# Kernel optimization log

Measured on AMD Instinct MI355X. Metric: run time of the kernel, lower is better.

Reference implementation:

```python
import jax, jax.numpy as jnp
import numpy as np

TEMPERATURE = 0.05


def setup_inputs() -> dict:
    key = jax.random.key(0)
    k1, k2 = jax.random.split(key)
    B, D = 4096, 1024
    # scale 0.1 keeps pairwise distances O(3) so the original exp(-d/T) is sane
    text_embeddings = 0.1 * jax.random.normal(k1, (B, D), dtype=jnp.float32)
    image_embeddings = 0.1 * jax.random.normal(k2, (B, D), dtype=jnp.float32)
    positive_pairs = jnp.arange(B, dtype=jnp.int32)  # unused by the loss body
    return {
        "text_embeddings": text_embeddings,
        "image_embeddings": image_embeddings,
        "positive_pairs": positive_pairs,
    }


def _pairwise_l2(t, m):
    # ||t_i - m_j|| via GEMM expansion; [B, B]
    sq = (
        jnp.sum(t * t, axis=1, keepdims=True)
        + jnp.sum(m * m, axis=1)[None, :]
        - 2.0 * (t @ m.T)
    )
    return jnp.sqrt(jnp.maximum(sq, 0.0))


def reference(text_embeddings, image_embeddings, positive_pairs):
    # loss_i = -log( exp(-d_ii/T) / sum_{j != i} exp(-d_ij/T) )
    #        = logsumexp_{j != i}(-d_ij/T) + d_ii/T   (exact same math, stable)
    dist = _pairwise_l2(text_embeddings, image_embeddings)  # [B, B]
    logits = -dist / TEMPERATURE
    diag = jnp.diagonal(logits)  # log numerator per row
    B = logits.shape[0]
    eye = jnp.eye(B, dtype=bool)
    masked = jnp.where(eye, -jnp.inf, logits)  # exclude self-term from denom
    lse = jax.nn.logsumexp(masked, axis=1)
    return jnp.mean(lse - diag)
```

## Files before the change

kernel.cpp:

```cpp
#include <hip/hip_runtime.h>
#include <math.h>


#define NB 4096
#define ND 1024
#define LSE_BIAS 90.0f
#define A2 28.85390082f
#define C2 129.8425537f

typedef short short8 __attribute__((ext_vector_type(8)));
typedef unsigned short ushort4v __attribute__((ext_vector_type(4)));
typedef float f32x4 __attribute__((ext_vector_type(4)));

__device__ inline unsigned short f2bf(float f) {
  unsigned int u = __float_as_uint(f);
  u = (u + 0x7FFFu + ((u >> 16) & 1u)) >> 16;
  return (unsigned short)u;
}

__device__ inline void gload_lds16(const unsigned short* g, unsigned short* l) {
  __builtin_amdgcn_global_load_lds(
      (const __attribute__((address_space(1))) unsigned int*)g,
      (__attribute__((address_space(3))) unsigned int*)l, 16, 0, 0);
}

__global__ void prep_kernel(const float* __restrict__ T, const float* __restrict__ M,
                            unsigned short* __restrict__ tb, unsigned short* __restrict__ mb,
                            float* __restrict__ tn, float* __restrict__ mn) {
  int row = blockIdx.x;
  const float* src;
  unsigned short* dst;
  float* nout;
  int r;
  if (row < NB) { src = T; dst = tb; nout = tn; r = row; }
  else          { src = M; dst = mb; nout = mn; r = row - NB; }
  float4 v = ((const float4*)(src + (size_t)r * ND))[threadIdx.x];
  float s = v.x * v.x + v.y * v.y + v.z * v.z + v.w * v.w;
  ushort4v o;
  o.x = f2bf(v.x); o.y = f2bf(v.y); o.z = f2bf(v.z); o.w = f2bf(v.w);
  *(ushort4v*)(dst + (size_t)r * ND + threadIdx.x * 4) = o;
  for (int off = 32; off; off >>= 1) s += __shfl_xor(s, off);
  __shared__ float wsum[4];
  if ((threadIdx.x & 63) == 0) wsum[threadIdx.x >> 6] = s;
  __syncthreads();
  if (threadIdx.x == 0) nout[r] = wsum[0] + wsum[1] + wsum[2] + wsum[3];
}

__launch_bounds__(256)
__global__ void gemm_lse_kernel(const unsigned short* __restrict__ tb,
                                const unsigned short* __restrict__ mb,
                                const float* __restrict__ tn, const float* __restrict__ mn,
                                float* __restrict__ part_s, float* __restrict__ diag) {
  __shared__ unsigned short Al[128 * 64];
  __shared__ unsigned short Bl[128 * 64];
  int rt = blockIdx.x, ct = blockIdx.y;
  int tid = threadIdx.x;
  int wave = tid >> 6, lane = tid & 63, quad = lane >> 4, l15 = lane & 15;
  int l8 = lane & 7, lr = lane >> 3;

  f32x4 acc[4][4] = {};

  int srow = wave * 32 + lr;
  int sc = l8 ^ lr;
  const unsigned short* gA = tb + (size_t)(rt * 128 + srow) * ND + sc * 8;
  const unsigned short* gB = mb + (size_t)(ct * 128 + srow) * ND + sc * 8;
  unsigned short* lA = Al + wave * 2048;
  unsigned short* lB = Bl + wave * 2048;

  int wr0 = (wave >> 1) * 64, wc0 = (wave & 1) * 64;
  int arow = (wr0 + l15) * 64;
  int brow = (wc0 + l15) * 64;
  int swz = quad ^ (l15 & 7);

  for (int kt = 0; kt < ND / 64; ++kt) {
#pragma unroll
    for (int i = 0; i < 4; ++i) {
      gload_lds16(gA + (size_t)i * 8 * ND, lA + i * 512);
      gload_lds16(gB + (size_t)i * 8 * ND, lB + i * 512);
    }
    __syncthreads();
#pragma unroll
    for (int kk = 0; kk < 2; ++kk) {
      int j8 = (swz ^ (kk << 2)) * 8;
      short8 af[4], bf[4];
#pragma unroll
      for (int f = 0; f < 4; ++f) {
        af[f] = *(const short8*)&Al[arow + f * 1024 + j8];
        bf[f] = *(const short8*)&Bl[brow + f * 1024 + j8];
      }
#pragma unroll
      for (int fr = 0; fr < 4; ++fr)
#pragma unroll
        for (int fc = 0; fc < 4; ++fc)
          acc[fr][fc] =
              __builtin_amdgcn_mfma_f32_16x16x32_bf16(af[fr], bf[fc], acc[fr][fc], 0, 0, 0);
    }
    __syncthreads();
    gA += 64;
    gB += 64;
  }

  int chunk = ct * 2 + (wave & 1);
  bool diagblk = (rt == ct);
  float mnv[4];
#pragma unroll
  for (int fc = 0; fc < 4; ++fc) mnv[fc] = mn[ct * 128 + wc0 + fc * 16 + l15];
#pragma unroll
  for (int fr = 0; fr < 4; ++fr) {
#pragma unroll
    for (int r = 0; r < 4; ++r) {
      int grow = rt * 128 + wr0 + fr * 16 + quad * 4 + r;
      float tnr = tn[grow];
      float s = 0.0f;
#pragma unroll
      for (int fc = 0; fc < 4; ++fc) {
        float sq = fmaxf(fmaf(-2.0f, acc[fr][fc][r], tnr + mnv[fc]), 0.0f);
        float droot = __builtin_amdgcn_sqrtf(sq);
        float e = __builtin_amdgcn_exp2f(fmaf(droot, -A2, C2));
        if (diagblk) {
          int gcol = ct * 128 + wc0 + fc * 16 + l15;
          if (grow == gcol) {
            diag[grow] = -20.0f * droot;
            e = 0.0f;
          }
        }
        s += e;
      }
      for (int m = 8; m; m >>= 1) s += __shfl_xor(s, m);
      if (l15 == 0) part_s[(size_t)grow * 64 + chunk] = s;
    }
  }
}

__global__ void combine_kernel(const float* __restrict__ part_s,
                               const float* __restrict__ diag, float* __restrict__ bsums) {
  int row = blockIdx.x * 256 + threadIdx.x;
  const float* ps = part_s + (size_t)row * 64;
  float S = 0.0f;
#pragma unroll 8
  for (int c = 0; c < 64; ++c) S += ps[c];
  float loss = (logf(S) - LSE_BIAS) - diag[row];
  for (int off = 32; off; off >>= 1) loss += __shfl_xor(loss, off);
  __shared__ float wsum[4];
  if ((threadIdx.x & 63) == 0) wsum[threadIdx.x >> 6] = loss;
  __syncthreads();
  if (threadIdx.x == 0) bsums[blockIdx.x] = wsum[0] + wsum[1] + wsum[2] + wsum[3];
}

__global__ void final_kernel(const float* __restrict__ bsums, float* __restrict__ out) {
  float s = (threadIdx.x < 16) ? bsums[threadIdx.x] : 0.0f;
  for (int off = 8; off; off >>= 1) s += __shfl_xor(s, off);
  if (threadIdx.x == 0) out[0] = s * (1.0f / (float)NB);
}

extern "C" void kernel_launch(void* const* d_in, const int* in_sizes, int n_in,
                              void* d_out, int out_size, void* d_ws, size_t ws_size,
                              hipStream_t stream) {
  const float* T = (const float*)d_in[0];
  const float* M = (const float*)d_in[1];
  float* out = (float*)d_out;

  unsigned short* tb = (unsigned short*)d_ws;
  unsigned short* mb = tb + (size_t)NB * ND;
  float* fbase = (float*)(mb + (size_t)NB * ND);
  float* tn = fbase;
  float* mn = tn + NB;
  float* diag = mn + NB;
  float* part_s = diag + NB;
  float* bsums = part_s + (size_t)NB * 64;

  prep_kernel<<<2 * NB, 256, 0, stream>>>(T, M, tb, mb, tn, mn);
  dim3 grid(NB / 128, NB / 128);
  gemm_lse_kernel<<<grid, 256, 0, stream>>>(tb, mb, tn, mn, part_s, diag);
  combine_kernel<<<NB / 256, 256, 0, stream>>>(part_s, diag, bsums);
  final_kernel<<<1, 64, 0, stream>>>(bsums, out);
}
```

Before: 129.9 us.

## Fuse row-sum combine and final reduction into GEMM via atomics and last-block pattern

Per-row partial exp sums are now accumulated into a single row-sum array with float atomicAdd instead of being written into a 64-wide partial buffer. The last GEMM block to finish, detected with a global counter, then computes the log, subtracts the diagonal and reduces to the mean. The accumulator and counter are zeroed in the prep kernel. This drops two kernel launches and the partial-buffer traffic, at the cost of atomic contention (64 adds per row) and float summation that is no longer deterministic.

```diff
diff --git a/kernel.cpp b/kernel.cpp
--- a/kernel.cpp
+++ b/kernel.cpp
@@ -7,6 +7,7 @@
 #define LSE_BIAS 90.0f
 #define A2 28.85390082f
 #define C2 129.8425537f
+#define LN2 0.6931471805599453f
 
 typedef short short8 __attribute__((ext_vector_type(8)));
 typedef unsigned short ushort4v __attribute__((ext_vector_type(4)));
@@ -26,8 +27,12 @@
 
 __global__ void prep_kernel(const float* __restrict__ T, const float* __restrict__ M,
                             unsigned short* __restrict__ tb, unsigned short* __restrict__ mb,
-                            float* __restrict__ tn, float* __restrict__ mn) {
+                            float* __restrict__ tn, float* __restrict__ mn,
+                            float* __restrict__ S, unsigned int* __restrict__ cnt) {
   int row = blockIdx.x;
+  if (row < 16) S[row * 256 + threadIdx.x] = 0.0f;
+  if (row == 16 && threadIdx.x == 0) *cnt = 0u;
+
   const float* src;
   unsigned short* dst;
   float* nout;
@@ -50,9 +55,11 @@
 __global__ void gemm_lse_kernel(const unsigned short* __restrict__ tb,
                                 const unsigned short* __restrict__ mb,
                                 const float* __restrict__ tn, const float* __restrict__ mn,
-                                float* __restrict__ part_s, float* __restrict__ diag) {
+                                float* __restrict__ S, float* __restrict__ diag,
+                                unsigned int* __restrict__ cnt, float* __restrict__ out) {
   __shared__ unsigned short Al[128 * 64];
   __shared__ unsigned short Bl[128 * 64];
+  __shared__ unsigned int lastFlag;
   int rt = blockIdx.x, ct = blockIdx.y;
   int tid = threadIdx.x;
   int wave = tid >> 6, lane = tid & 63, quad = lane >> 4, l15 = lane & 15;
@@ -100,7 +107,6 @@
     gB += 64;
   }
 
-  int chunk = ct * 2 + (wave & 1);
   bool diagblk = (rt == ct);
   float mnv[4];
 #pragma unroll
@@ -127,30 +133,34 @@
         s += e;
       }
       for (int m = 8; m; m >>= 1) s += __shfl_xor(s, m);
-      if (l15 == 0) part_s[(size_t)grow * 64 + chunk] = s;
+      if (l15 == 0) atomicAdd(&S[grow], s);
     }
   }
-}
 
-__global__ void combine_kernel(const float* __restrict__ part_s,
-                               const float* __restrict__ diag, float* __restrict__ bsums) {
-  int row = blockIdx.x * 256 + threadIdx.x;
-  const float* ps = part_s + (size_t)row * 64;
-  float S = 0.0f;
-#pragma unroll 8
-  for (int c = 0; c < 64; ++c) S += ps[c];
-  float loss = (logf(S) - LSE_BIAS) - diag[row];
-  for (int off = 32; off; off >>= 1) loss += __shfl_xor(loss, off);
-  __shared__ float wsum[4];
-  if ((threadIdx.x & 63) == 0) wsum[threadIdx.x >> 6] = loss;
+  __threadfence();
   __syncthreads();
-  if (threadIdx.x == 0) bsums[blockIdx.x] = wsum[0] + wsum[1] + wsum[2] + wsum[3];
-}
-
-__global__ void final_kernel(const float* __restrict__ bsums, float* __restrict__ out) {
-  float s = (threadIdx.x < 16) ? bsums[threadIdx.x] : 0.0f;
-  for (int off = 8; off; off >>= 1) s += __shfl_xor(s, off);
-  if (threadIdx.x == 0) out[0] = s * (1.0f / (float)NB);
+  if (tid == 0) {
+    unsigned int old = atomicAdd(cnt, 1u);
+    lastFlag = (old == 1023u) ? 1u : 0u;
+  }
+  __syncthreads();
+  if (lastFlag) {
+    __threadfence();
+    float accv = 0.0f;
+#pragma unroll
+    for (int i = 0; i < 16; ++i) {
+      int row = i * 256 + tid;
+      float Sv = S[row];
+      float loss = LN2 * __builtin_amdgcn_logf(Sv) - LSE_BIAS - diag[row];
+      accv += loss;
+    }
+    for (int off = 32; off; off >>= 1) accv += __shfl_xor(accv, off);
+    float* wsum = (float*)Al;
+    __syncthreads();
+    if ((tid & 63) == 0) wsum[tid >> 6] = accv;
+    __syncthreads();
+    if (tid == 0) out[0] = (wsum[0] + wsum[1] + wsum[2] + wsum[3]) * (1.0f / (float)NB);
+  }
 }
 
 extern "C" void kernel_launch(void* const* d_in, const int* in_sizes, int n_in,
@@ -166,12 +176,10 @@
   float* tn = fbase;
   float* mn = tn + NB;
   float* diag = mn + NB;
-  float* part_s = diag + NB;
-  float* bsums = part_s + (size_t)NB * 64;
+  float* S = diag + NB;
+  unsigned int* cnt = (unsigned int*)(S + NB);
 
-  prep_kernel<<<2 * NB, 256, 0, stream>>>(T, M, tb, mb, tn, mn);
+  prep_kernel<<<2 * NB, 256, 0, stream>>>(T, M, tb, mb, tn, mn, S, cnt);
   dim3 grid(NB / 128, NB / 128);
-  gemm_lse_kernel<<<grid, 256, 0, stream>>>(tb, mb, tn, mn, part_s, diag);
-  combine_kernel<<<NB / 256, 256, 0, stream>>>(part_s, diag, bsums);
-  final_kernel<<<1, 64, 0, stream>>>(bsums, out);
+  gemm_lse_kernel<<<grid, 256, 0, stream>>>(tb, mb, tn, mn, S, diag, cnt, out);
 }
```

Measured after the change: 186.5 us. +43.6%, slower.

## Switch GEMM from bf16 to fp8 using scaled 32x32x64 MFMA

Applied to the files above, without the earlier changes.

Converts the embeddings to fp8 (e4m3) in the prep kernel instead of bf16 and runs the distance GEMM with the MX-scaled 32x32x64 f8f6f4 MFMA using unit scales. K tiles grow to 128 bytes, the LDS layout and swizzle are reworked, the epilogue is remapped to the 32x32 accumulator layout, and launch bounds request 4 blocks per SM. This halves operand bytes and doubles MFMA throughput, but fp8 rounding of the dot products adds error to distances that are scaled by 1/T inside the exponent. Combine also switches to the hardware log2 intrinsic.

```diff
diff --git a/kernel.cpp b/kernel.cpp
--- a/kernel.cpp
+++ b/kernel.cpp
@@ -7,38 +7,34 @@
 #define LSE_BIAS 90.0f
 #define A2 28.85390082f
 #define C2 129.8425537f
+#define LN2 0.6931471805599453f
+#define SCALE1 0x7F7F7F7Fu
 
-typedef short short8 __attribute__((ext_vector_type(8)));
-typedef unsigned short ushort4v __attribute__((ext_vector_type(4)));
-typedef float f32x4 __attribute__((ext_vector_type(4)));
+typedef int v8i __attribute__((ext_vector_type(8)));
+typedef int int4v __attribute__((ext_vector_type(4)));
+typedef float v16f __attribute__((ext_vector_type(16)));
 
-__device__ inline unsigned short f2bf(float f) {
-  unsigned int u = __float_as_uint(f);
-  u = (u + 0x7FFFu + ((u >> 16) & 1u)) >> 16;
-  return (unsigned short)u;
-}
-
-__device__ inline void gload_lds16(const unsigned short* g, unsigned short* l) {
+__device__ inline void gload_lds16(const unsigned char* g, unsigned char* l) {
   __builtin_amdgcn_global_load_lds(
       (const __attribute__((address_space(1))) unsigned int*)g,
       (__attribute__((address_space(3))) unsigned int*)l, 16, 0, 0);
 }
 
 __global__ void prep_kernel(const float* __restrict__ T, const float* __restrict__ M,
-                            unsigned short* __restrict__ tb, unsigned short* __restrict__ mb,
+                            unsigned char* __restrict__ t8, unsigned char* __restrict__ m8,
                             float* __restrict__ tn, float* __restrict__ mn) {
   int row = blockIdx.x;
   const float* src;
-  unsigned short* dst;
+  unsigned char* dst;
   float* nout;
   int r;
-  if (row < NB) { src = T; dst = tb; nout = tn; r = row; }
-  else          { src = M; dst = mb; nout = mn; r = row - NB; }
+  if (row < NB) { src = T; dst = t8; nout = tn; r = row; }
+  else          { src = M; dst = m8; nout = mn; r = row - NB; }
   float4 v = ((const float4*)(src + (size_t)r * ND))[threadIdx.x];
   float s = v.x * v.x + v.y * v.y + v.z * v.z + v.w * v.w;
-  ushort4v o;
-  o.x = f2bf(v.x); o.y = f2bf(v.y); o.z = f2bf(v.z); o.w = f2bf(v.w);
-  *(ushort4v*)(dst + (size_t)r * ND + threadIdx.x * 4) = o;
+  int p = __builtin_amdgcn_cvt_pk_fp8_f32(v.x, v.y, 0, false);
+  p = __builtin_amdgcn_cvt_pk_fp8_f32(v.z, v.w, p, true);
+  ((int*)(dst + (size_t)r * ND))[threadIdx.x] = p;
   for (int off = 32; off; off >>= 1) s += __shfl_xor(s, off);
   __shared__ float wsum[4];
   if ((threadIdx.x & 63) == 0) wsum[threadIdx.x >> 6] = s;
@@ -46,88 +42,91 @@
   if (threadIdx.x == 0) nout[r] = wsum[0] + wsum[1] + wsum[2] + wsum[3];
 }
 
-__launch_bounds__(256)
-__global__ void gemm_lse_kernel(const unsigned short* __restrict__ tb,
-                                const unsigned short* __restrict__ mb,
+__launch_bounds__(256, 4)
+__global__ void gemm_lse_kernel(const unsigned char* __restrict__ t8,
+                                const unsigned char* __restrict__ m8,
                                 const float* __restrict__ tn, const float* __restrict__ mn,
                                 float* __restrict__ part_s, float* __restrict__ diag) {
-  __shared__ unsigned short Al[128 * 64];
-  __shared__ unsigned short Bl[128 * 64];
+  __shared__ unsigned char Al[128 * 128];
+  __shared__ unsigned char Bl[128 * 128];
   int rt = blockIdx.x, ct = blockIdx.y;
   int tid = threadIdx.x;
-  int wave = tid >> 6, lane = tid & 63, quad = lane >> 4, l15 = lane & 15;
-  int l8 = lane & 7, lr = lane >> 3;
+  int wave = tid >> 6, lane = tid & 63;
+  int hb = lane >> 5, l31 = lane & 31;
 
-  f32x4 acc[4][4] = {};
+  v16f acc[2][2] = {};
 
-  int srow = wave * 32 + lr;
-  int sc = l8 ^ lr;
-  const unsigned short* gA = tb + (size_t)(rt * 128 + srow) * ND + sc * 8;
-  const unsigned short* gB = mb + (size_t)(ct * 128 + srow) * ND + sc * 8;
-  unsigned short* lA = Al + wave * 2048;
-  unsigned short* lB = Bl + wave * 2048;
+  int l3 = lane >> 3;
+  int gc = (lane & 7) ^ l3;
+  const unsigned char* gA = t8 + (size_t)(rt * 128 + wave * 32 + l3) * ND + gc * 16;
+  const unsigned char* gB = m8 + (size_t)(ct * 128 + wave * 32 + l3) * ND + gc * 16;
+  unsigned char* lA = Al + wave * 4096;
+  unsigned char* lB = Bl + wave * 4096;
 
   int wr0 = (wave >> 1) * 64, wc0 = (wave & 1) * 64;
-  int arow = (wr0 + l15) * 64;
-  int brow = (wc0 + l15) * 64;
-  int swz = quad ^ (l15 & 7);
+  int sw = l31 & 7;
+  int abase = (wr0 + l31) * 128;
+  int bbase = (wc0 + l31) * 128;
 
-  for (int kt = 0; kt < ND / 64; ++kt) {
+  for (int kt = 0; kt < ND / 128; ++kt) {
 #pragma unroll
     for (int i = 0; i < 4; ++i) {
-      gload_lds16(gA + (size_t)i * 8 * ND, lA + i * 512);
-      gload_lds16(gB + (size_t)i * 8 * ND, lB + i * 512);
+      gload_lds16(gA + (size_t)i * 8 * ND, lA + i * 1024);
+      gload_lds16(gB + (size_t)i * 8 * ND, lB + i * 1024);
     }
     __syncthreads();
 #pragma unroll
-    for (int kk = 0; kk < 2; ++kk) {
-      int j8 = (swz ^ (kk << 2)) * 8;
-      short8 af[4], bf[4];
+    for (int ks = 0; ks < 2; ++ks) {
+      int q = (ks * 4 + 2 * hb) ^ sw;
+      union { v8i v; int4v h[2]; } af[2], bf[2];
 #pragma unroll
-      for (int f = 0; f < 4; ++f) {
-        af[f] = *(const short8*)&Al[arow + f * 1024 + j8];
-        bf[f] = *(const short8*)&Bl[brow + f * 1024 + j8];
+      for (int f = 0; f < 2; ++f) {
+        af[f].h[0] = *(const int4v*)&Al[abase + f * 4096 + q * 16];
+        af[f].h[1] = *(const int4v*)&Al[abase + f * 4096 + (q ^ 1) * 16];
+        bf[f].h[0] = *(const int4v*)&Bl[bbase + f * 4096 + q * 16];
+        bf[f].h[1] = *(const int4v*)&Bl[bbase + f * 4096 + (q ^ 1) * 16];
       }
 #pragma unroll
-      for (int fr = 0; fr < 4; ++fr)
+      for (int fr = 0; fr < 2; ++fr)
 #pragma unroll
-        for (int fc = 0; fc < 4; ++fc)
-          acc[fr][fc] =
-              __builtin_amdgcn_mfma_f32_16x16x32_bf16(af[fr], bf[fc], acc[fr][fc], 0, 0, 0);
+        for (int fc = 0; fc < 2; ++fc)
+          acc[fr][fc] = __builtin_amdgcn_mfma_scale_f32_32x32x64_f8f6f4(
+              af[fr].v, bf[fc].v, acc[fr][fc], 0, 0, 0, SCALE1, 0, SCALE1);
     }
     __syncthreads();
-    gA += 64;
-    gB += 64;
+    gA += 128;
+    gB += 128;
   }
 
   int chunk = ct * 2 + (wave & 1);
   bool diagblk = (rt == ct);
-  float mnv[4];
+  float mnv[2];
 #pragma unroll
-  for (int fc = 0; fc < 4; ++fc) mnv[fc] = mn[ct * 128 + wc0 + fc * 16 + l15];
+  for (int fc = 0; fc < 2; ++fc) mnv[fc] = mn[ct * 128 + wc0 + fc * 32 + l31];
 #pragma unroll
-  for (int fr = 0; fr < 4; ++fr) {
+  for (int fr = 0; fr < 2; ++fr) {
 #pragma unroll
-    for (int r = 0; r < 4; ++r) {
-      int grow = rt * 128 + wr0 + fr * 16 + quad * 4 + r;
+    for (int reg = 0; reg < 16; ++reg) {
+      int row = (reg & 3) + 8 * (reg >> 2) + 4 * hb;
+      int grow = rt * 128 + wr0 + fr * 32 + row;
       float tnr = tn[grow];
       float s = 0.0f;
 #pragma unroll
-      for (int fc = 0; fc < 4; ++fc) {
-        float sq = fmaxf(fmaf(-2.0f, acc[fr][fc][r], tnr + mnv[fc]), 0.0f);
-        float droot = __builtin_amdgcn_sqrtf(sq);
-        float e = __builtin_amdgcn_exp2f(fmaf(droot, -A2, C2));
+      for (int fc = 0; fc < 2; ++fc) {
+        float sq = fmaxf(fmaf(-2.0f, acc[fr][fc][reg], tnr + mnv[fc]), 0.0f);
+        float dr = __builtin_amdgcn_sqrtf(sq);
+        float e = __builtin_amdgcn_exp2f(fmaf(dr, -A2, C2));
         if (diagblk) {
-          int gcol = ct * 128 + wc0 + fc * 16 + l15;
+          int gcol = ct * 128 + wc0 + fc * 32 + l31;
           if (grow == gcol) {
-            diag[grow] = -20.0f * droot;
+            diag[grow] = -20.0f * dr;
             e = 0.0f;
           }
         }
         s += e;
       }
-      for (int m = 8; m; m >>= 1) s += __shfl_xor(s, m);
-      if (l15 == 0) part_s[(size_t)grow * 64 + chunk] = s;
+      for (int m = 16; m; m >>= 1) s += __shfl_xor(s, m);
+      if (l31 == 0) part_s[(size_t)grow * 64 + chunk] = s;
     }
   }
 }
@@ -139,7 +138,7 @@
   float S = 0.0f;
 #pragma unroll 8
   for (int c = 0; c < 64; ++c) S += ps[c];
-  float loss = (logf(S) - LSE_BIAS) - diag[row];
+  float loss = (LN2 * __builtin_amdgcn_logf(S) - LSE_BIAS) - diag[row];
   for (int off = 32; off; off >>= 1) loss += __shfl_xor(loss, off);
   __shared__ float wsum[4];
   if ((threadIdx.x & 63) == 0) wsum[threadIdx.x >> 6] = loss;
@@ -160,18 +159,18 @@
   const float* M = (const float*)d_in[1];
   float* out = (float*)d_out;
 
-  unsigned short* tb = (unsigned short*)d_ws;
-  unsigned short* mb = tb + (size_t)NB * ND;
-  float* fbase = (float*)(mb + (size_t)NB * ND);
+  unsigned char* t8 = (unsigned char*)d_ws;
+  unsigned char* m8 = t8 + (size_t)NB * ND;
+  float* fbase = (float*)(m8 + (size_t)NB * ND);
   float* tn = fbase;
   float* mn = tn + NB;
   float* diag = mn + NB;
   float* part_s = diag + NB;
   float* bsums = part_s + (size_t)NB * 64;
 
-  prep_kernel<<<2 * NB, 256, 0, stream>>>(T, M, tb, mb, tn, mn);
+  prep_kernel<<<2 * NB, 256, 0, stream>>>(T, M, t8, m8, tn, mn);
   dim3 grid(NB / 128, NB / 128);
-  gemm_lse_kernel<<<grid, 256, 0, stream>>>(tb, mb, tn, mn, part_s, diag);
+  gemm_lse_kernel<<<grid, 256, 0, stream>>>(t8, m8, tn, mn, part_s, diag);
   combine_kernel<<<NB / 256, 256, 0, stream>>>(part_s, diag, bsums);
   final_kernel<<<1, 64, 0, stream>>>(bsums, out);
 }
```

After: 263.7 us. +102.9%, slower.
